# Kernel tuning notes

Hardware: AMD Instinct MI355X
Metric: run time of the kernel (lower is better)

Reference implementation:

```python
import jax, jax.numpy as jnp
import numpy as np

NUM_HEADS = 16


def setup_inputs() -> dict:
    key = jax.random.key(0)
    k1, k2, k3 = jax.random.split(key, 3)
    b, d, s = 2, 1024, 2048
    x = jax.random.normal(k1, (b, d, s), dtype=jnp.float32)
    # torch nn.Linear(d, 3d) without bias == x @ W1 with W1 of shape (d, 3d)
    W1 = jax.random.normal(k2, (d, 3 * d), dtype=jnp.float32) * (d ** -0.5)
    W2 = jax.random.normal(k3, (d, d), dtype=jnp.float32) * (d ** -0.5)
    return {"x": x, "W1": W1, "W2": W2}


def reference(x, W1, W2):
    # x: (b, hidden_dim, s) -> (b, s, hidden_dim)
    b, d, s = x.shape
    h = NUM_HEADS
    hd = d // h
    xt = jnp.swapaxes(x, 1, 2)                       # (b, s, d)
    qkv = xt @ W1                                    # (b, s, 3d)
    qkv = qkv.reshape(b, s, 3, h, hd)
    qkv = jnp.transpose(qkv, (2, 0, 3, 1, 4))        # (3, b, h, s, hd)
    q, k, v = qkv[0], qkv[1], qkv[2]
    scale = hd ** -0.5
    scores = jnp.einsum("bhqd,bhkd->bhqk", q, k) * scale  # (b, h, s, s)
    # causal mask: same as torch code (adds float32 min where not lower-tri)
    neg = jnp.finfo(jnp.float32).min
    causal = jnp.tril(jnp.ones((s, s), dtype=bool))
    scores = jnp.where(causal[None, None, :, :], scores, scores + neg)
    attn = jax.nn.softmax(scores, axis=-1)           # dropout = identity (eval)
    out = jnp.einsum("bhqk,bhkd->bhqd", attn, v)     # (b, h, s, hd)
    out = jnp.transpose(out, (0, 2, 1, 3)).reshape(b, s, d)
    out = out @ W2                                   # (b, s, d)
    return jnp.swapaxes(out, 1, 2)                   # (b, d, s)
```

## Files before the change

kernel.cpp:

```cpp
#include <hip/hip_runtime.h>
#include <math.h>

#define B_  2
#define D_  1024
#define S_  2048
#define H_  16
#define HD_ 64
#define D3_ 3072
#define M_  4096

typedef __attribute__((ext_vector_type(8))) short short8;
typedef __attribute__((ext_vector_type(4))) float float4v;

__device__ __forceinline__ short f2bf(float f) {
    unsigned u = __builtin_bit_cast(unsigned, f);
    unsigned r = (u + 0x7FFFu + ((u >> 16) & 1u)) >> 16;
    return (short)r;
}

__device__ __forceinline__ unsigned cvt_pk_bf16(float lo, float hi) {
    unsigned r;
    asm("v_cvt_pk_bf16_f32 %0, %1, %2" : "=v"(r) : "v"(lo), "v"(hi));
    return r;
}

__device__ __forceinline__ float fast_exp2(float x) {
    float r;
    asm("v_exp_f32 %0, %1" : "=v"(r) : "v"(x));
    return r;
}

#define GLD16(gsrc, ldst)                                                      \
    __builtin_amdgcn_global_load_lds(                                          \
        (const __attribute__((address_space(1))) void*)(gsrc),                 \
        (__attribute__((address_space(3))) void*)(ldst), 16, 0, 0)

__global__ __launch_bounds__(256) void transpose_cvt(const float* __restrict__ in,
                                                     short* __restrict__ out,
                                                     int R, int C) {
    __shared__ float t[32][33];
    const int c0 = blockIdx.x * 32, r0 = blockIdx.y * 32;
    const float* inb = in + (size_t)blockIdx.z * R * C;
    short* outb = out + (size_t)blockIdx.z * R * C;
    const int tx = threadIdx.x, ty = threadIdx.y;
    #pragma unroll
    for (int i = ty; i < 32; i += 8)
        t[i][tx] = inb[(size_t)(r0 + i) * C + c0 + tx];
    __syncthreads();
    #pragma unroll
    for (int i = ty; i < 32; i += 8)
        outb[(size_t)(c0 + i) * R + r0 + tx] = f2bf(t[tx][i]);
}

__device__ __forceinline__ void gemm_core(const short* __restrict__ A,
                                          const short* __restrict__ Bt,
                                          int m0, int n0,
                                          short* As, short* Bs,
                                          float4v acc[4][4]) {
    const int tid = threadIdx.x;
    const int lane = tid & 63, w = tid >> 6;
    const int wr = (w >> 1) * 64, wc = (w & 1) * 64;
    const int srow = lane >> 2;
    const int scol = ((lane & 3) ^ ((srow >> 1) & 3)) * 8;
    const int rr = lane & 15;
    const int kc = ((lane >> 4) ^ ((rr >> 1) & 3)) * 8;
    for (int k0 = 0; k0 < 1024; k0 += 32) {
        #pragma unroll
        for (int j = 0; j < 2; ++j) {
            const int ch = 2 * w + j;
            GLD16(A  + (size_t)(m0 + ch * 16 + srow) * 1024 + k0 + scol,
                  As + ch * 512 + lane * 8);
            GLD16(Bt + (size_t)(n0 + ch * 16 + srow) * 1024 + k0 + scol,
                  Bs + ch * 512 + lane * 8);
        }
        __syncthreads();
        short8 a[4], b[4];
        #pragma unroll
        for (int m = 0; m < 4; ++m)
            a[m] = *(const short8*)&As[(wr + m * 16 + rr) * 32 + kc];
        #pragma unroll
        for (int n = 0; n < 4; ++n)
            b[n] = *(const short8*)&Bs[(wc + n * 16 + rr) * 32 + kc];
        #pragma unroll
        for (int m = 0; m < 4; ++m)
            #pragma unroll
            for (int n = 0; n < 4; ++n)
                acc[m][n] = __builtin_amdgcn_mfma_f32_16x16x32_bf16(a[m], b[n], acc[m][n], 0, 0, 0);
        __syncthreads();
    }
}

__global__ __launch_bounds__(256) void gemm_qkv_mfma(const short* __restrict__ xt,
                                                     const short* __restrict__ W1t,
                                                     short* __restrict__ q,
                                                     short* __restrict__ kk,
                                                     short* __restrict__ vt) {
    __shared__ short As[128 * 32], Bs[128 * 32];
    float4v acc[4][4];
    #pragma unroll
    for (int m = 0; m < 4; ++m)
        #pragma unroll
        for (int n = 0; n < 4; ++n) acc[m][n] = (float4v){0.f, 0.f, 0.f, 0.f};
    const int m0 = blockIdx.y * 128, n0 = blockIdx.x * 128;
    gemm_core(xt, W1t, m0, n0, As, Bs, acc);
    const int lane = threadIdx.x & 63, w = threadIdx.x >> 6;
    const int wr = (w >> 1) * 64, wc = (w & 1) * 64;
    const float qscale = 0.125f * 1.44269504f;
    #pragma unroll
    for (int n = 0; n < 4; ++n) {
        const int gcol = n0 + wc + n * 16 + (lane & 15);
        const int which = gcol >> 10, hh = (gcol >> 6) & 15, hd = gcol & 63;
        #pragma unroll
        for (int m = 0; m < 4; ++m) {
            #pragma unroll
            for (int ri = 0; ri < 4; ++ri) {
                const int grow = m0 + wr + m * 16 + (lane >> 4) * 4 + ri;
                const int bb = grow >> 11, ss = grow & (S_ - 1);
                float av = acc[m][n][ri];
                if (which == 0) av *= qscale;
                const short v = f2bf(av);
                if (which == 0)      q [((size_t)(bb * H_ + hh) * S_ + ss) * HD_ + hd] = v;
                else if (which == 1) kk[((size_t)(bb * H_ + hh) * S_ + ss) * HD_ + hd] = v;
                else                 vt[((size_t)(bb * H_ + hh) * HD_ + hd) * S_ + ss] = v;
            }
        }
    }
}

__global__ __launch_bounds__(256) void attn_mfma(const short* __restrict__ q,
                                                 const short* __restrict__ k,
                                                 const short* __restrict__ vt,
                                                 short* __restrict__ ao) {
    __shared__ short Ks[2][64 * 64];
    __shared__ short Vts[2][64 * 64];
    __shared__ short Ps[64 * 64];
    __shared__ float sums[64];
    const int tid = threadIdx.x;
    const int lane = tid & 63, w = tid >> 6;
    const int bid = (int)blockIdx.x;
    const int xcd = bid & 7, slot = bid >> 3;
    const int bh = xcd * 4 + (slot & 3);
    const int qpair = slot >> 2;
    const size_t base = (size_t)bh * S_ * HD_;
    const short* qp = q + base;
    const short* kp = k + base;
    const short* vp = vt + base;
    const int bb = bh >> 4, hh = bh & 15;
    const int wrow = w * 16;

    for (int half = 0; half < 2; ++half) {
        const int qt = (half == 0) ? qpair : 31 - qpair;
        const int q0 = qt * 64;
        short8 qf[2];
        #pragma unroll
        for (int ks = 0; ks < 2; ++ks)
            qf[ks] = *(const short8*)&qp[(size_t)(q0 + wrow + (lane & 15)) * HD_
                                         + ks * 32 + (lane >> 4) * 8];
        float4v accO[4];
        float lsum = 0.f;
        #pragma unroll
        for (int n = 0; n < 4; ++n) accO[n] = (float4v){0.f, 0.f, 0.f, 0.f};

        const int nkb = qt + 1;
        __syncthreads();
        #pragma unroll
        for (int j = 0; j < 2; ++j) {
            const int g = (w * 2 + j) * 64 + lane;
            const int r = g >> 3, cs = g & 7;
            const int co = (cs ^ (r & 7)) << 3;
            GLD16(kp + (size_t)r * HD_ + co, &Ks[0][g * 8]);
            GLD16(vp + (size_t)r * S_ + co,  &Vts[0][g * 8]);
        }
        int cur = 0;
        for (int kb = 0; kb < nkb; ++kb) {
            const int kv0 = kb * 64;
            __syncthreads();
            if (kb + 1 < nkb) {
                const int kv1 = kv0 + 64;
                #pragma unroll
                for (int j = 0; j < 2; ++j) {
                    const int g = (w * 2 + j) * 64 + lane;
                    const int r = g >> 3, cs = g & 7;
                    const int co = (cs ^ (r & 7)) << 3;
                    GLD16(kp + (size_t)(kv1 + r) * HD_ + co, &Ks[cur ^ 1][g * 8]);
                    GLD16(vp + (size_t)r * S_ + kv1 + co,    &Vts[cur ^ 1][g * 8]);
                }
            }
            float4v accS[4];
            #pragma unroll
            for (int n = 0; n < 4; ++n) accS[n] = (float4v){0.f, 0.f, 0.f, 0.f};
            #pragma unroll
            for (int ks = 0; ks < 2; ++ks) {
                #pragma unroll
                for (int n = 0; n < 4; ++n) {
                    const int rowk = n * 16 + (lane & 15);
                    const int ch = ks * 4 + (lane >> 4);
                    const short8 kf = *(const short8*)&Ks[cur][rowk * 64 + ((ch ^ (rowk & 7)) << 3)];
                    accS[n] = __builtin_amdgcn_mfma_f32_16x16x32_bf16(kf, qf[ks], accS[n], 0, 0, 0);
                }
            }
            const bool diag = (kb == qt);
            const int qg = q0 + wrow + (lane & 15);
            const int prow = wrow + (lane & 15);
            #pragma unroll
            for (int n = 0; n < 4; ++n) {
                const int kvb = kv0 + n * 16 + ((lane >> 4) << 2);
                float p[4];
                if (diag) {
                    const int dlim = qg - kvb;
                    #pragma unroll
                    for (int ri = 0; ri < 4; ++ri)
                        p[ri] = (ri <= dlim) ? fast_exp2(accS[n][ri]) : 0.f;
                } else {
                    #pragma unroll
                    for (int ri = 0; ri < 4; ++ri)
                        p[ri] = fast_exp2(accS[n][ri]);
                }
                lsum += (p[0] + p[1]) + (p[2] + p[3]);
                const unsigned lo = cvt_pk_bf16(p[0], p[1]);
                const unsigned hi = cvt_pk_bf16(p[2], p[3]);
                const int col = n * 16 + ((lane >> 4) << 2);
                const int ch = col >> 3;
                const int addr = prow * 64 + ((ch ^ (prow & 7)) << 3) + (col & 7);
                *(uint2*)&Ps[addr] = (uint2){lo, hi};
            }
            #pragma unroll
            for (int ks = 0; ks < 2; ++ks) {
                const int prow2 = wrow + (lane & 15);
                const int chp = ks * 4 + (lane >> 4);
                const short8 pf = *(const short8*)&Ps[prow2 * 64 + ((chp ^ (prow2 & 7)) << 3)];
                #pragma unroll
                for (int n = 0; n < 4; ++n) {
                    const int vrow = n * 16 + (lane & 15);
                    const int ch = ks * 4 + (lane >> 4);
                    const short8 vf = *(const short8*)&Vts[cur][vrow * 64 + ((ch ^ (vrow & 7)) << 3)];
                    accO[n] = __builtin_amdgcn_mfma_f32_16x16x32_bf16(pf, vf, accO[n], 0, 0, 0);
                }
            }
            cur ^= 1;
        }
        {
            float t = lsum;
            t += __shfl_xor(t, 16);
            t += __shfl_xor(t, 32);
            if (lane < 16) sums[wrow + lane] = t;
        }
        #pragma unroll
        for (int ri = 0; ri < 4; ++ri) {
            const int lrow = wrow + ((lane >> 4) << 2) + ri;
            const float inv = 1.f / sums[lrow];
            const int grow = q0 + lrow;
            #pragma unroll
            for (int n = 0; n < 4; ++n) {
                const int col = hh * 64 + n * 16 + (lane & 15);
                ao[((size_t)(bb * S_ + grow)) * D_ + col] = f2bf(accO[n][ri] * inv);
            }
        }
    }
}

__global__ __launch_bounds__(256) void gemm_out_mfma(const short* __restrict__ W2t,
                                                     const short* __restrict__ ao,
                                                     float* __restrict__ out) {
    __shared__ short As[128 * 32], Bs[128 * 32];
    float4v acc[4][4];
    #pragma unroll
    for (int m = 0; m < 4; ++m)
        #pragma unroll
        for (int n = 0; n < 4; ++n) acc[m][n] = (float4v){0.f, 0.f, 0.f, 0.f};
    const int m0 = blockIdx.y * 128, n0 = blockIdx.x * 128;
    gemm_core(W2t, ao, m0, n0, As, Bs, acc);
    const int lane = threadIdx.x & 63, w = threadIdx.x >> 6;
    const int wr = (w >> 1) * 64, wc = (w & 1) * 64;
    #pragma unroll
    for (int m = 0; m < 4; ++m) {
        #pragma unroll
        for (int ri = 0; ri < 4; ++ri) {
            const int grow = m0 + wr + m * 16 + (lane >> 4) * 4 + ri;
            #pragma unroll
            for (int n = 0; n < 4; ++n) {
                const int gcol = n0 + wc + n * 16 + (lane & 15);
                const int bb = gcol >> 11, ss = gcol & (S_ - 1);
                out[(size_t)bb * D_ * S_ + (size_t)grow * S_ + ss] = acc[m][n][ri];
            }
        }
    }
}

extern "C" void kernel_launch(void* const* d_in, const int* in_sizes, int n_in,
                              void* d_out, int out_size, void* d_ws, size_t ws_size,
                              hipStream_t stream) {
    const float* x  = (const float*)d_in[0];
    const float* W1 = (const float*)d_in[1];
    const float* W2 = (const float*)d_in[2];
    float* out = (float*)d_out;

    short* xt  = (short*)d_ws;
    short* W1t = xt  + (size_t)M_ * D_;
    short* W2t = W1t + (size_t)D3_ * D_;
    short* q   = W2t + (size_t)D_ * D_;
    short* kk  = q   + (size_t)B_ * H_ * S_ * HD_;
    short* vt  = kk  + (size_t)B_ * H_ * S_ * HD_;
    short* ao  = vt  + (size_t)B_ * H_ * S_ * HD_;

    transpose_cvt<<<dim3(S_ / 32, D_ / 32, B_), dim3(32, 8), 0, stream>>>(x, xt, D_, S_);
    transpose_cvt<<<dim3(D3_ / 32, D_ / 32, 1), dim3(32, 8), 0, stream>>>(W1, W1t, D_, D3_);
    transpose_cvt<<<dim3(D_ / 32, D_ / 32, 1), dim3(32, 8), 0, stream>>>(W2, W2t, D_, D_);
    gemm_qkv_mfma<<<dim3(D3_ / 128, M_ / 128), 256, 0, stream>>>(xt, W1t, q, kk, vt);
    attn_mfma<<<dim3(512), 256, 0, stream>>>(q, kk, vt, ao);
    gemm_out_mfma<<<dim3(M_ / 128, D_ / 128), 256, 0, stream>>>(W2t, ao, out);
}
```

Before: 120.7 us.

## Fuse three transpose-convert launches into one and remap QKV GEMM blocks per XCD

The three separate fp32-to-bf16 transpose kernels become one launch that picks x, W1 or W2 from the block index. It uses 64x64 tiles, float2 loads, short2 stores and a bf16 shared-memory tile, which cuts launch overhead and halves shared-memory traffic. The QKV GEMM grid is flattened to 1D and remapped so that each XCD (block index mod 8) handles a contiguous 8x12 tile region, aiming to improve L2 reuse of A and B panels. The risks are branch divergence in the fused kernel and possible shared-memory bank conflicts in the transposed short reads.

```diff
diff --git a/kernel.cpp b/kernel.cpp
--- a/kernel.cpp
+++ b/kernel.cpp
@@ -35,21 +35,50 @@
         (const __attribute__((address_space(1))) void*)(gsrc),                 \
         (__attribute__((address_space(3))) void*)(ldst), 16, 0, 0)
 
-__global__ __launch_bounds__(256) void transpose_cvt(const float* __restrict__ in,
-                                                     short* __restrict__ out,
-                                                     int R, int C) {
-    __shared__ float t[32][33];
-    const int c0 = blockIdx.x * 32, r0 = blockIdx.y * 32;
-    const float* inb = in + (size_t)blockIdx.z * R * C;
-    short* outb = out + (size_t)blockIdx.z * R * C;
-    const int tx = threadIdx.x, ty = threadIdx.y;
-    #pragma unroll
-    for (int i = ty; i < 32; i += 8)
-        t[i][tx] = inb[(size_t)(r0 + i) * C + c0 + tx];
+__global__ __launch_bounds__(256) void transpose_cvt_all(const float* __restrict__ x,
+                                                         short* __restrict__ xt,
+                                                         const float* __restrict__ W1,
+                                                         short* __restrict__ W1t,
+                                                         const float* __restrict__ W2,
+                                                         short* __restrict__ W2t) {
+    __shared__ short t[64][66];
+    const int bid = (int)blockIdx.x;
+    const float* in;
+    short* out;
+    int C, R, rb, cb;
+    if (bid < 1024) {
+        const int z = bid >> 9, tt = bid & 511;
+        R = D_; C = S_;
+        cb = tt & 31; rb = tt >> 5;
+        in = x + (size_t)z * D_ * S_;
+        out = xt + (size_t)z * D_ * S_;
+    } else if (bid < 1792) {
+        const int tt = bid - 1024;
+        R = D_; C = D3_;
+        cb = tt % 48; rb = tt / 48;
+        in = W1; out = W1t;
+    } else {
+        const int tt = bid - 1792;
+        R = D_; C = D_;
+        cb = tt & 15; rb = tt >> 4;
+        in = W2; out = W2t;
+    }
+    const int r0 = rb * 64, c0 = cb * 64;
+    const int tx = threadIdx.x & 31, ty = threadIdx.x >> 5;
+    #pragma unroll
+    for (int i = ty; i < 64; i += 8) {
+        const float2 v = *(const float2*)&in[(size_t)(r0 + i) * C + c0 + tx * 2];
+        t[i][tx * 2]     = f2bf(v.x);
+        t[i][tx * 2 + 1] = f2bf(v.y);
+    }
     __syncthreads();
     #pragma unroll
-    for (int i = ty; i < 32; i += 8)
-        outb[(size_t)(c0 + i) * R + r0 + tx] = f2bf(t[tx][i]);
+    for (int j = ty; j < 64; j += 8) {
+        short2 v;
+        v.x = t[tx * 2][j];
+        v.y = t[tx * 2 + 1][j];
+        *(short2*)&out[(size_t)(c0 + j) * R + r0 + tx * 2] = v;
+    }
 }
 
 __device__ __forceinline__ void gemm_core(const short* __restrict__ A,
@@ -101,7 +130,11 @@
     for (int m = 0; m < 4; ++m)
         #pragma unroll
         for (int n = 0; n < 4; ++n) acc[m][n] = (float4v){0.f, 0.f, 0.f, 0.f};
-    const int m0 = blockIdx.y * 128, n0 = blockIdx.x * 128;
+    const int bid = (int)blockIdx.x;
+    const int xcd = bid & 7, r = bid >> 3;
+    const int mt = (xcd & 3) * 8 + (r & 7);
+    const int nt = (xcd >> 2) * 12 + (r >> 3);
+    const int m0 = mt * 128, n0 = nt * 128;
     gemm_core(xt, W1t, m0, n0, As, Bs, acc);
     const int lane = threadIdx.x & 63, w = threadIdx.x >> 6;
     const int wr = (w >> 1) * 64, wc = (w & 1) * 64;
@@ -303,10 +336,8 @@
     short* vt  = kk  + (size_t)B_ * H_ * S_ * HD_;
     short* ao  = vt  + (size_t)B_ * H_ * S_ * HD_;
 
-    transpose_cvt<<<dim3(S_ / 32, D_ / 32, B_), dim3(32, 8), 0, stream>>>(x, xt, D_, S_);
-    transpose_cvt<<<dim3(D3_ / 32, D_ / 32, 1), dim3(32, 8), 0, stream>>>(W1, W1t, D_, D3_);
-    transpose_cvt<<<dim3(D_ / 32, D_ / 32, 1), dim3(32, 8), 0, stream>>>(W2, W2t, D_, D_);
-    gemm_qkv_mfma<<<dim3(D3_ / 128, M_ / 128), 256, 0, stream>>>(xt, W1t, q, kk, vt);
+    transpose_cvt_all<<<dim3(2048), 256, 0, stream>>>(x, xt, W1, W1t, W2, W2t);
+    gemm_qkv_mfma<<<dim3(768), 256, 0, stream>>>(xt, W1t, q, kk, vt);
     attn_mfma<<<dim3(512), 256, 0, stream>>>(q, kk, vt, ao);
     gemm_out_mfma<<<dim3(M_ / 128, D_ / 128), 256, 0, stream>>>(W2t, ao, out);
 }
```

After: 114.3 us. -5.3%, faster.
